# Performance work log

Measured on AMD Instinct MI355X. Metric: run time of the kernel, lower is better.

The kernel has to match this reference:

```python
import jax, jax.numpy as jnp
import numpy as np

DIM_Q = 512
DIM_K = 512
DIM_V = 512
NUM_HEADS = 8
TEMPERATURE = 0.1
LN_EPS = 1e-5


def setup_inputs() -> dict:
    key = jax.random.key(0)
    ks = jax.random.split(key, 12)
    B, n_q, n_k = 8, 1024, 1024
    s = 0.02
    return {
        "Q": jax.random.normal(ks[0], (B, n_q, DIM_Q), jnp.float32),
        "K": jax.random.normal(ks[1], (B, n_k, DIM_K), jnp.float32),
        "mask": jnp.ones((B, n_k), dtype=bool),
        "Wq": jax.random.normal(ks[2], (DIM_Q, DIM_V), jnp.float32) * s,
        "bq": jnp.zeros((DIM_V,), jnp.float32),
        "Wk": jax.random.normal(ks[3], (DIM_K, DIM_V), jnp.float32) * s,
        "bk": jnp.zeros((DIM_V,), jnp.float32),
        "Wv": jax.random.normal(ks[4], (DIM_K, DIM_V), jnp.float32) * s,
        "bv": jnp.zeros((DIM_V,), jnp.float32),
        "Wo": jax.random.normal(ks[5], (DIM_V, DIM_V), jnp.float32) * s,
        "bo": jnp.zeros((DIM_V,), jnp.float32),
        "gamma": jnp.ones((DIM_V,), jnp.float32),
        "beta": jnp.zeros((DIM_V,), jnp.float32),
    }


def _mab(Q, K, mask, Wq, bq, Wk, bk, Wv, bv, Wo, bo, gamma, beta):
    B, n_q, _ = Q.shape
    n_k = K.shape[1]
    H = NUM_HEADS
    d_head = DIM_V // H
    # projections, split heads: [B, H, n, d_head]
    Qh = (Q @ Wq + bq).reshape(B, n_q, H, d_head).transpose(0, 2, 1, 3)
    Kh = (K @ Wk + bk).reshape(B, n_k, H, d_head).transpose(0, 2, 1, 3)
    Vh = (K @ Wv + bv).reshape(B, n_k, H, d_head).transpose(0, 2, 1, 3)
    scale = 1.0 / (np.sqrt(d_head) * TEMPERATURE)
    A = jnp.einsum("bhqd,bhkd->bhqk", Qh, Kh) * scale
    A = jnp.where(mask[:, None, None, :], A, -jnp.inf)
    A = jax.nn.softmax(A, axis=-1)
    O = jnp.einsum("bhqk,bhkd->bhqd", A, Vh)
    O = O.transpose(0, 2, 1, 3).reshape(B, n_q, DIM_V)
    # fused output FFN + residual + LN
    O = O + jax.nn.relu(O @ Wo + bo)
    mu = jnp.mean(O, axis=-1, keepdims=True)
    var = jnp.var(O, axis=-1, keepdims=True)
    return (O - mu) * jax.lax.rsqrt(var + LN_EPS) * gamma + beta


def reference(Q, K, mask, Wq, bq, Wk, bk, Wv, bv, Wo, bo, gamma, beta):
    return _mab(Q, K, mask, Wq, bq, Wk, bk, Wv, bv, Wo, bo, gamma, beta)
```

## Files before the change

kernel.cpp:

```cpp
#include <hip/hip_runtime.h>

typedef __bf16 bf16;
typedef bf16 bf16x4 __attribute__((ext_vector_type(4)));
typedef bf16 bf16x8 __attribute__((ext_vector_type(8)));
typedef float floatx4 __attribute__((ext_vector_type(4)));

#define NB 8
#define NQ 1024
#define NK 1024
#define DIM 512
#define NH 8
#define DH 64

__device__ __forceinline__ void async16(const void* g, void* l) {
    __builtin_amdgcn_global_load_lds(
        (const __attribute__((address_space(1))) unsigned int*)(unsigned long long)(g),
        (__attribute__((address_space(3))) unsigned int*)(unsigned long long)(l),
        16, 0, 0);
}

__global__ __launch_bounds__(256) void prep_fused(
    const float* __restrict__ Q, const float* __restrict__ K,
    const float* __restrict__ Wq, const float* __restrict__ Wk,
    const float* __restrict__ Wv, const float* __restrict__ Wo,
    bf16* __restrict__ Qb, bf16* __restrict__ Kb, bf16* __restrict__ Wt)
{
    __shared__ bf16 Tl[64][68];
    const int bid = blockIdx.x;
    if (bid < 4096) {
        const int i = bid * 256 + threadIdx.x;
        float4 a = ((const float4*)Q)[i];
        float4 c = ((const float4*)K)[i];
        bf16x4 qa = {(bf16)a.x, (bf16)a.y, (bf16)a.z, (bf16)a.w};
        bf16x4 ka = {(bf16)c.x, (bf16)c.y, (bf16)c.z, (bf16)c.w};
        *(bf16x4*)(Qb + (size_t)i * 4) = qa;
        *(bf16x4*)(Kb + (size_t)i * 4) = ka;
    } else {
        const int bid2 = bid - 4096;
        const int w = bid2 >> 6;
        const int bx = bid2 & 7, by = (bid2 >> 3) & 7;
        const float* W = (w == 0) ? Wq : (w == 1) ? Wk : (w == 2) ? Wv : Wo;
        bf16* out = Wt + (size_t)w * DIM * DIM;
        const int k0 = bx * 64, n0 = by * 64;
        const int tx = threadIdx.x & 15, ty = threadIdx.x >> 4;
        for (int pass = 0; pass < 4; ++pass) {
            int k = ty + pass * 16;
            float4 v = *(const float4*)&W[(size_t)(k0 + k) * DIM + n0 + tx * 4];
            Tl[tx * 4 + 0][k] = (bf16)v.x;
            Tl[tx * 4 + 1][k] = (bf16)v.y;
            Tl[tx * 4 + 2][k] = (bf16)v.z;
            Tl[tx * 4 + 3][k] = (bf16)v.w;
        }
        __syncthreads();
        for (int pass = 0; pass < 4; ++pass) {
            int n = ty + pass * 16;
            bf16x4 ov = *(const bf16x4*)&Tl[n][tx * 4];
            *(bf16x4*)&out[(size_t)(n0 + n) * DIM + k0 + tx * 4] = ov;
        }
    }
}

__global__ __launch_bounds__(256) void proj_fused(
    const bf16* __restrict__ Qb, const bf16* __restrict__ Kb,
    const bf16* __restrict__ Wt,
    const float* __restrict__ bq, const float* __restrict__ bk,
    const float* __restrict__ bv,
    bf16* __restrict__ Qp, bf16* __restrict__ Kp, bf16* __restrict__ Vpt)
{
    __shared__ __attribute__((aligned(16))) bf16 sh[24576];
    const int t = threadIdx.x;
    const int wave = t >> 6, lane = t & 63, quad = lane >> 4, l16 = lane & 15;
    const int wr = wave >> 1, wc = wave & 1;
    const int bid = blockIdx.x;
    const bool isQ = bid < 512;
    const bf16* A; const bf16* W; int m0, n0;
    if (isQ) { A = Qb; W = Wt;             m0 = (bid & 63) * 128;  n0 = (bid >> 6) * 64; }
    else     { int b2 = bid - 512;
               A = Kb; W = Wt + 512 * DIM; m0 = (b2 & 63) * 128;   n0 = (b2 >> 6) * 64; }

    const int r1 = t >> 3, s1 = t & 7;
    const int p1 = s1 ^ (r1 & 7);
    const bf16* aSrc = A + (size_t)(m0 + r1) * DIM + p1 * 8;
    const bf16* wSrc = W + (size_t)(n0 + r1) * DIM + p1 * 8;

    floatx4 acc[4][2];
    for (int i = 0; i < 4; ++i)
        for (int j = 0; j < 2; ++j) acc[i][j] = (floatx4){0.f, 0.f, 0.f, 0.f};

    #pragma unroll
    for (int j = 0; j < 4; ++j)
        async16(aSrc + (size_t)j * 32 * DIM, sh + (t + j * 256) * 8);
    #pragma unroll
    for (int j = 0; j < 2; ++j)
        async16(wSrc + (size_t)j * 32 * DIM, sh + 16384 + (t + j * 256) * 8);

    for (int kt = 0; kt < 8; ++kt) {
        __syncthreads();
        const int cur = kt & 1;
        bf16* Acur = sh + cur * 8192;
        bf16* Bcur = sh + 16384 + cur * 4096;
        if (kt < 7) {
            bf16* Anxt = sh + (1 - cur) * 8192;
            bf16* Bnxt = sh + 16384 + (1 - cur) * 4096;
            const int ko = (kt + 1) * 64;
            #pragma unroll
            for (int j = 0; j < 4; ++j)
                async16(aSrc + ko + (size_t)j * 32 * DIM, Anxt + (t + j * 256) * 8);
            #pragma unroll
            for (int j = 0; j < 2; ++j)
                async16(wSrc + ko + (size_t)j * 32 * DIM, Bnxt + (t + j * 256) * 8);
        }
        #pragma unroll
        for (int ks = 0; ks < 2; ++ks) {
            bf16x8 af[4], bfr[2];
            #pragma unroll
            for (int mi = 0; mi < 4; ++mi) {
                const int row = wr * 64 + mi * 16 + l16;
                af[mi] = *(const bf16x8*)(Acur + row * 64 + (((ks * 4 + quad) ^ (row & 7)) << 3));
            }
            #pragma unroll
            for (int ni = 0; ni < 2; ++ni) {
                const int row = wc * 32 + ni * 16 + l16;
                bfr[ni] = *(const bf16x8*)(Bcur + row * 64 + (((ks * 4 + quad) ^ (row & 7)) << 3));
            }
            #pragma unroll
            for (int mi = 0; mi < 4; ++mi)
                #pragma unroll
                for (int ni = 0; ni < 2; ++ni)
                    acc[mi][ni] = __builtin_amdgcn_mfma_f32_16x16x32_bf16(
                        af[mi], bfr[ni], acc[mi][ni], 0, 0, 0);
        }
    }

    const bool isV = (!isQ) && (n0 >= 512);
    if (!isV) {
        bf16* out = isQ ? Qp : Kp;
        const float* bias = isQ ? bq : bk;
        const float qscale = isQ ? 1.8033688f : 1.0f;
        for (int ni = 0; ni < 2; ++ni) {
            const int n = n0 + wc * 32 + ni * 16 + l16;
            const float bb = bias[n];
            const int hd = n >> 6, d = n & 63;
            for (int mi = 0; mi < 4; ++mi) {
                for (int r = 0; r < 4; ++r) {
                    const int m = m0 + wr * 64 + mi * 16 + quad * 4 + r;
                    const int b = m >> 10, q = m & 1023;
                    out[((size_t)(b * 8 + hd) * 1024 + q) * 64 + d] =
                        (bf16)((acc[mi][ni][r] + bb) * qscale);
                }
            }
        }
    } else {
        __syncthreads();
        for (int ni = 0; ni < 2; ++ni) {
            const int n = wc * 32 + ni * 16 + l16;
            const float bb = bv[n0 + n - 512];
            for (int mi = 0; mi < 4; ++mi) {
                const int mb = wr * 64 + mi * 16 + quad * 4;
                const int slot = ((mb >> 3) ^ (n & 15));
                bf16x4 pk = {(bf16)(acc[mi][ni][0] + bb), (bf16)(acc[mi][ni][1] + bb),
                             (bf16)(acc[mi][ni][2] + bb), (bf16)(acc[mi][ni][3] + bb)};
                *(bf16x4*)(sh + n * 128 + slot * 8 + (mb & 7)) = pk;
            }
        }
        __syncthreads();
        const int n = t >> 2, hf = t & 3;
        const int nv = n0 + n - 512, hd = nv >> 6, d = nv & 63;
        const int b = m0 >> 10, qb = m0 & 1023;
        bf16* dst = Vpt + ((size_t)(b * 8 + hd) * 64 + d) * 1024 + qb;
        #pragma unroll
        for (int j = 0; j < 4; ++j) {
            const int ch = hf * 4 + j;
            const int slot = ch ^ (n & 15);
            bf16x8 v8 = *(const bf16x8*)(sh + n * 128 + slot * 8);
            *(bf16x8*)(dst + ch * 8) = v8;
        }
    }
}

__global__ __launch_bounds__(256, 4) void attn_kernel(
    const bf16* __restrict__ Qp, const bf16* __restrict__ Kp,
    const bf16* __restrict__ Vpt, const int* __restrict__ mask,
    bf16* __restrict__ Oa)
{
    const int bh = blockIdx.x & 63, qblk = blockIdx.x >> 6;
    const int b = bh >> 3, hd = bh & 7;
    const int t = threadIdx.x;
    const int wave = t >> 6, lane = t & 63, quad = lane >> 4, l16 = lane & 15;
    const int wq = wave >> 1, wk = wave & 1;

    __shared__ __attribute__((aligned(16))) bf16 Kt[2][64 * 64];
    __shared__ __attribute__((aligned(16))) bf16 Vt[2][64 * 64];
    __shared__ __attribute__((aligned(16))) bf16 Pl[4][32 * 32];

    const bf16* Qbase = Qp + ((size_t)bh * NQ + qblk * 64 + wq * 32) * DH;
    const bf16* Kbase = Kp + (size_t)bh * NK * DH;
    const bf16* Vbase = Vpt + (size_t)bh * DH * NK;
    const int* mrow = mask + b * NK;

    bf16x8 qf[2][2];
    #pragma unroll
    for (int qg = 0; qg < 2; ++qg)
        #pragma unroll
        for (int hh = 0; hh < 2; ++hh)
            qf[qg][hh] = *(const bf16x8*)(Qbase + (size_t)(qg * 16 + l16) * DH + hh * 32 + quad * 8);

    bf16x8 onesv;
    #pragma unroll
    for (int j = 0; j < 8; ++j) onesv[j] = (bf16)1.0f;

    floatx4 o[2][4];
    floatx4 osum[2];
    #pragma unroll
    for (int qg = 0; qg < 2; ++qg) {
        osum[qg] = (floatx4){0.f, 0.f, 0.f, 0.f};
        #pragma unroll
        for (int i = 0; i < 4; ++i) o[qg][i] = (floatx4){0.f, 0.f, 0.f, 0.f};
    }

    const int r1 = t >> 3, s1 = t & 7;
    const int p1 = s1 ^ (r1 & 7);
    const bf16* kSrc = Kbase + r1 * 64 + p1 * 8;
    const bf16* vSrc = Vbase + (size_t)r1 * 1024 + p1 * 8;

    async16(kSrc, Kt[0] + t * 8);
    async16(kSrc + 32 * 64, Kt[0] + (t + 256) * 8);
    async16(vSrc, Vt[0] + t * 8);
    async16(vSrc + (size_t)32 * 1024, Vt[0] + (t + 256) * 8);

    const int xor3 = (l16 & 3) ^ ((l16 >> 2) & 3);

    for (int kt = 0; kt < NK / 64; ++kt) {
        __syncthreads();
        const int cur = kt & 1;
        if (kt < NK / 64 - 1) {
            const int nxt = 1 - cur;
            async16(kSrc + (kt + 1) * 4096, Kt[nxt] + t * 8);
            async16(kSrc + (kt + 1) * 4096 + 32 * 64, Kt[nxt] + (t + 256) * 8);
            async16(vSrc + (kt + 1) * 64, Vt[nxt] + t * 8);
            async16(vSrc + (kt + 1) * 64 + (size_t)32 * 1024, Vt[nxt] + (t + 256) * 8);
        }

        bf16x8 kb[2][2];
        #pragma unroll
        for (int sub = 0; sub < 2; ++sub) {
            const int rowk = wk * 32 + sub * 16 + l16;
            kb[sub][0] = *(const bf16x8*)(Kt[cur] + rowk * 64 + ((quad ^ (rowk & 7)) << 3));
            kb[sub][1] = *(const bf16x8*)(Kt[cur] + rowk * 64 + (((quad + 4) ^ (rowk & 7)) << 3));
        }
        floatx4 sf[2][2];
        __builtin_amdgcn_s_setprio(1);
        #pragma unroll
        for (int sub = 0; sub < 2; ++sub)
            #pragma unroll
            for (int qg = 0; qg < 2; ++qg) {
                floatx4 s = {0.f, 0.f, 0.f, 0.f};
                s = __builtin_amdgcn_mfma_f32_16x16x32_bf16(kb[sub][0], qf[qg][0], s, 0, 0, 0);
                s = __builtin_amdgcn_mfma_f32_16x16x32_bf16(kb[sub][1], qf[qg][1], s, 0, 0, 0);
                sf[sub][qg] = s;
            }
        __builtin_amdgcn_s_setprio(0);

        const int mv = mrow[kt * 64 + lane];
        if (!__all(mv != 0)) {
            #pragma unroll
            for (int sub = 0; sub < 2; ++sub) {
                const int4 m4 = *(const int4*)&mrow[kt * 64 + wk * 32 + sub * 16 + quad * 4];
                #pragma unroll
                for (int qg = 0; qg < 2; ++qg) {
                    if (!m4.x) sf[sub][qg][0] = -3.0e38f;
                    if (!m4.y) sf[sub][qg][1] = -3.0e38f;
                    if (!m4.z) sf[sub][qg][2] = -3.0e38f;
                    if (!m4.w) sf[sub][qg][3] = -3.0e38f;
                }
            }
        }
        #pragma unroll
        for (int sub = 0; sub < 2; ++sub)
            #pragma unroll
            for (int qg = 0; qg < 2; ++qg) {
                bf16x4 pk = {(bf16)__builtin_amdgcn_exp2f(sf[sub][qg][0]),
                             (bf16)__builtin_amdgcn_exp2f(sf[sub][qg][1]),
                             (bf16)__builtin_amdgcn_exp2f(sf[sub][qg][2]),
                             (bf16)__builtin_amdgcn_exp2f(sf[sub][qg][3])};
                const int slot = (sub * 2 + (quad >> 1)) ^ xor3;
                *(bf16x4*)&Pl[wave][(qg * 16 + l16) * 32 + slot * 8 + (quad & 1) * 4] = pk;
            }
        bf16x8 af[2];
        #pragma unroll
        for (int qg = 0; qg < 2; ++qg)
            af[qg] = *(const bf16x8*)&Pl[wave][(qg * 16 + l16) * 32 + ((quad ^ xor3) << 3)];

        __builtin_amdgcn_s_setprio(1);
        osum[0] = __builtin_amdgcn_mfma_f32_16x16x32_bf16(af[0], onesv, osum[0], 0, 0, 0);
        osum[1] = __builtin_amdgcn_mfma_f32_16x16x32_bf16(af[1], onesv, osum[1], 0, 0, 0);
        #pragma unroll
        for (int dsub = 0; dsub < 4; ++dsub) {
            const int d = dsub * 16 + l16;
            bf16x8 vb = *(const bf16x8*)(Vt[cur] + d * 64 + (((wk * 4 + quad) ^ (d & 7)) << 3));
            o[0][dsub] = __builtin_amdgcn_mfma_f32_16x16x32_bf16(af[0], vb, o[0][dsub], 0, 0, 0);
            o[1][dsub] = __builtin_amdgcn_mfma_f32_16x16x32_bf16(af[1], vb, o[1][dsub], 0, 0, 0);
        }
        __builtin_amdgcn_s_setprio(0);
    }

    __syncthreads();
    float* scr  = (float*)Kt;
    float* scrL = (float*)Vt;

    {
        float* reg = scr + wave * 1024;
        if (wk == 0) {
            #pragma unroll
            for (int dsub = 0; dsub < 4; ++dsub)
                *(floatx4*)(reg + dsub * 256 + lane * 4) = o[1][dsub];
            if (l16 == 0) {
                #pragma unroll
                for (int r = 0; r < 4; ++r)
                    scrL[wave * 16 + quad * 4 + r] = osum[1][r];
            }
        } else {
            #pragma unroll
            for (int dsub = 0; dsub < 4; ++dsub)
                *(floatx4*)(reg + dsub * 256 + lane * 4) = o[0][dsub];
            if (l16 == 0) {
                #pragma unroll
                for (int r = 0; r < 4; ++r)
                    scrL[wave * 16 + quad * 4 + r] = osum[0][r];
            }
        }
    }
    __syncthreads();
    {
        const int partner = wq * 2 + (1 - wk);
        float* reg = scr + partner * 1024;
        floatx4 oo[4];
        floatx4 os;
        if (wk == 0) {
            oo[0] = o[0][0]; oo[1] = o[0][1]; oo[2] = o[0][2]; oo[3] = o[0][3];
            os = osum[0];
        } else {
            oo[0] = o[1][0]; oo[1] = o[1][1]; oo[2] = o[1][2]; oo[3] = o[1][3];
            os = osum[1];
        }
        #pragma unroll
        for (int dsub = 0; dsub < 4; ++dsub)
            oo[dsub] += *(const floatx4*)(reg + dsub * 256 + lane * 4);
        float linv[4];
        #pragma unroll
        for (int r = 0; r < 4; ++r)
            linv[r] = 1.f / (os[r] + scrL[partner * 16 + quad * 4 + r]);
        for (int dsub = 0; dsub < 4; ++dsub) {
            for (int r = 0; r < 4; ++r) {
                const int q = qblk * 64 + wq * 32 + wk * 16 + quad * 4 + r;
                const int col = hd * 64 + dsub * 16 + l16;
                Oa[((size_t)(b * NQ + q)) * DIM + col] = (bf16)(oo[dsub][r] * linv[r]);
            }
        }
    }
}

__global__ __launch_bounds__(256) void ffn_gemm(
    const bf16* __restrict__ Oa, const bf16* __restrict__ W,
    const float* __restrict__ bias, bf16* __restrict__ Yb)
{
    __shared__ __attribute__((aligned(16))) bf16 sh[32768];
    const int t = threadIdx.x;
    const int wave = t >> 6, lane = t & 63, quad = lane >> 4, l16 = lane & 15;
    const int wr = wave >> 1, wc = wave & 1;
    const int m0 = (blockIdx.x & 63) * 128, n0 = (blockIdx.x >> 6) * 64;
    const int ktr = n0 >> 6;

    const int r1 = t >> 3, s1 = t & 7;
    const int p1 = s1 ^ (r1 & 7);
    const bf16* aSrc = Oa + (size_t)(m0 + r1) * DIM + p1 * 8;
    const bf16* wSrc = W  + (size_t)(n0 + r1) * DIM + p1 * 8;

    floatx4 acc[4][2];
    for (int i = 0; i < 4; ++i)
        for (int j = 0; j < 2; ++j) acc[i][j] = (floatx4){0.f, 0.f, 0.f, 0.f};

    #pragma unroll
    for (int j = 0; j < 4; ++j)
        async16(aSrc + (size_t)j * 32 * DIM, sh + (t + j * 256) * 8);
    #pragma unroll
    for (int j = 0; j < 2; ++j)
        async16(wSrc + (size_t)j * 32 * DIM, sh + 16384 + (t + j * 256) * 8);

    for (int kt = 0; kt < 8; ++kt) {
        __syncthreads();
        const int cur = kt & 1;
        bf16* Acur = sh + cur * 8192;
        bf16* Bcur = sh + 16384 + cur * 4096;
        if (kt < 7) {
            bf16* Anxt = sh + (1 - cur) * 8192;
            bf16* Bnxt = sh + 16384 + (1 - cur) * 4096;
            const int ko = (kt + 1) * 64;
            #pragma unroll
            for (int j = 0; j < 4; ++j)
                async16(aSrc + ko + (size_t)j * 32 * DIM, Anxt + (t + j * 256) * 8);
            #pragma unroll
            for (int j = 0; j < 2; ++j)
                async16(wSrc + ko + (size_t)j * 32 * DIM, Bnxt + (t + j * 256) * 8);
        }
        if (kt == ktr) {
            #pragma unroll
            for (int j = 0; j < 4; ++j) {
                const int idx = t + j * 256;
                *(bf16x8*)(sh + 24576 + idx * 8) = *(const bf16x8*)(Acur + idx * 8);
            }
        }
        #pragma unroll
        for (int ks = 0; ks < 2; ++ks) {
            bf16x8 af[4], bfr[2];
            #pragma unroll
            for (int mi = 0; mi < 4; ++mi) {
                const int row = wr * 64 + mi * 16 + l16;
                af[mi] = *(const bf16x8*)(Acur + row * 64 + (((ks * 4 + quad) ^ (row & 7)) << 3));
            }
            #pragma unroll
            for (int ni = 0; ni < 2; ++ni) {
                const int row = wc * 32 + ni * 16 + l16;
                bfr[ni] = *(const bf16x8*)(Bcur + row * 64 + (((ks * 4 + quad) ^ (row & 7)) << 3));
            }
            #pragma unroll
            for (int mi = 0; mi < 4; ++mi)
                #pragma unroll
                for (int ni = 0; ni < 2; ++ni)
                    acc[mi][ni] = __builtin_amdgcn_mfma_f32_16x16x32_bf16(
                        af[mi], bfr[ni], acc[mi][ni], 0, 0, 0);
        }
    }
    __syncthreads();

    for (int ni = 0; ni < 2; ++ni) {
        const int n = n0 + wc * 32 + ni * 16 + l16;
        const int cl = wc * 32 + ni * 16 + l16;
        const int chi = cl >> 3, clo = cl & 7;
        const float bb = bias[n];
        for (int mi = 0; mi < 4; ++mi) {
            for (int r = 0; r < 4; ++r) {
                const int rl = wr * 64 + mi * 16 + quad * 4 + r;
                const float ov = (float)sh[24576 + rl * 64 + ((chi ^ (rl & 7)) << 3) + clo];
                Yb[(size_t)(m0 + rl) * DIM + n] = (bf16)(ov + fmaxf(acc[mi][ni][r] + bb, 0.f));
            }
        }
    }
}

__global__ __launch_bounds__(256) void ln_kernel(
    const bf16* __restrict__ Y, const float* __restrict__ gamma,
    const float* __restrict__ beta, float* __restrict__ out)
{
    const int row  = blockIdx.x * 4 + (threadIdx.x >> 6);
    const int lane = threadIdx.x & 63;
    bf16x8 v = *(const bf16x8*)(Y + (size_t)row * DIM + lane * 8);
    float f[8];
    float s = 0.f, sq = 0.f;
    #pragma unroll
    for (int j = 0; j < 8; ++j) {
        f[j] = (float)v[j];
        s += f[j];
        sq += f[j] * f[j];
    }
    for (int mk = 32; mk >= 1; mk >>= 1) {
        s  += __shfl_xor(s,  mk, 64);
        sq += __shfl_xor(sq, mk, 64);
    }
    const float mu  = s * (1.f / 512.f);
    const float var = sq * (1.f / 512.f) - mu * mu;
    const float inv = rsqrtf(var + 1e-5f);
    float4 g1 = ((const float4*)gamma)[lane * 2];
    float4 g2 = ((const float4*)gamma)[lane * 2 + 1];
    float4 b1 = ((const float4*)beta)[lane * 2];
    float4 b2 = ((const float4*)beta)[lane * 2 + 1];
    float4 o1, o2;
    o1.x = (f[0] - mu) * inv * g1.x + b1.x;
    o1.y = (f[1] - mu) * inv * g1.y + b1.y;
    o1.z = (f[2] - mu) * inv * g1.z + b1.z;
    o1.w = (f[3] - mu) * inv * g1.w + b1.w;
    o2.x = (f[4] - mu) * inv * g2.x + b2.x;
    o2.y = (f[5] - mu) * inv * g2.y + b2.y;
    o2.z = (f[6] - mu) * inv * g2.z + b2.z;
    o2.w = (f[7] - mu) * inv * g2.w + b2.w;
    float* orow = out + (size_t)row * DIM;
    ((float4*)orow)[lane * 2]     = o1;
    ((float4*)orow)[lane * 2 + 1] = o2;
}

extern "C" void kernel_launch(void* const* d_in, const int* in_sizes, int n_in,
                              void* d_out, int out_size, void* d_ws, size_t ws_size,
                              hipStream_t stream) {
    const float* Q  = (const float*)d_in[0];
    const float* K  = (const float*)d_in[1];
    const int*   mask = (const int*)d_in[2];
    const float* Wq = (const float*)d_in[3];
    const float* bq = (const float*)d_in[4];
    const float* Wk = (const float*)d_in[5];
    const float* bk = (const float*)d_in[6];
    const float* Wv = (const float*)d_in[7];
    const float* bv = (const float*)d_in[8];
    const float* Wo = (const float*)d_in[9];
    const float* bo = (const float*)d_in[10];
    const float* gamma = (const float*)d_in[11];
    const float* beta  = (const float*)d_in[12];

    char* ws = (char*)d_ws;
    bf16* Wt  = (bf16*)(ws);
    bf16* Qb  = (bf16*)(ws + 2097152);
    bf16* Kb  = (bf16*)(ws + 10485760);
    bf16* Qp  = (bf16*)(ws + 18874368);
    bf16* Kp  = (bf16*)(ws + 27262976);
    bf16* Vpt = (bf16*)(ws + 35651584);
    bf16* Oa  = (bf16*)(ws + 44040192);
    bf16* Yb  = (bf16*)(ws + 52428800);
    float* out = (float*)d_out;

    prep_fused<<<4352, 256, 0, stream>>>(Q, K, Wq, Wk, Wv, Wo, Qb, Kb, Wt);
    proj_fused<<<1536, 256, 0, stream>>>(Qb, Kb, Wt, bq, bk, bv, Qp, Kp, Vpt);
    attn_kernel<<<1024, 256, 0, stream>>>(Qp, Kp, Vpt, mask, Oa);
    ffn_gemm<<<512, 256, 0, stream>>>(Oa, Wt + 3 * 262144, bo, Yb);
    ln_kernel<<<2048, 256, 0, stream>>>(Yb, gamma, beta, out);
}
```

Measured before the change: 162.5 us.

## Fuse fp32-to-bf16 conversion of Q and K into projection GEMM loads

Removes the separate elementwise pass that converted Q and K to bf16 in the workspace. The projection kernel now loads fp32 activation tiles into registers, converts them, and writes swizzled bf16 into shared memory, prefetching the next tile across the MFMA loop. This drops one full write plus re-read of 16 MB of intermediate data. In exchange the A-tile loads become synchronous register loads that take more VGPRs, and each K tile is reread as fp32 by the eight column blocks that share it.

```diff
diff --git a/kernel.cpp b/kernel.cpp
--- a/kernel.cpp
+++ b/kernel.cpp
@@ -20,48 +20,36 @@
 }
 
 __global__ __launch_bounds__(256) void prep_fused(
-    const float* __restrict__ Q, const float* __restrict__ K,
     const float* __restrict__ Wq, const float* __restrict__ Wk,
     const float* __restrict__ Wv, const float* __restrict__ Wo,
-    bf16* __restrict__ Qb, bf16* __restrict__ Kb, bf16* __restrict__ Wt)
+    bf16* __restrict__ Wt)
 {
     __shared__ bf16 Tl[64][68];
-    const int bid = blockIdx.x;
-    if (bid < 4096) {
-        const int i = bid * 256 + threadIdx.x;
-        float4 a = ((const float4*)Q)[i];
-        float4 c = ((const float4*)K)[i];
-        bf16x4 qa = {(bf16)a.x, (bf16)a.y, (bf16)a.z, (bf16)a.w};
-        bf16x4 ka = {(bf16)c.x, (bf16)c.y, (bf16)c.z, (bf16)c.w};
-        *(bf16x4*)(Qb + (size_t)i * 4) = qa;
-        *(bf16x4*)(Kb + (size_t)i * 4) = ka;
-    } else {
-        const int bid2 = bid - 4096;
-        const int w = bid2 >> 6;
-        const int bx = bid2 & 7, by = (bid2 >> 3) & 7;
-        const float* W = (w == 0) ? Wq : (w == 1) ? Wk : (w == 2) ? Wv : Wo;
-        bf16* out = Wt + (size_t)w * DIM * DIM;
-        const int k0 = bx * 64, n0 = by * 64;
-        const int tx = threadIdx.x & 15, ty = threadIdx.x >> 4;
-        for (int pass = 0; pass < 4; ++pass) {
-            int k = ty + pass * 16;
-            float4 v = *(const float4*)&W[(size_t)(k0 + k) * DIM + n0 + tx * 4];
-            Tl[tx * 4 + 0][k] = (bf16)v.x;
-            Tl[tx * 4 + 1][k] = (bf16)v.y;
-            Tl[tx * 4 + 2][k] = (bf16)v.z;
-            Tl[tx * 4 + 3][k] = (bf16)v.w;
-        }
-        __syncthreads();
-        for (int pass = 0; pass < 4; ++pass) {
-            int n = ty + pass * 16;
-            bf16x4 ov = *(const bf16x4*)&Tl[n][tx * 4];
-            *(bf16x4*)&out[(size_t)(n0 + n) * DIM + k0 + tx * 4] = ov;
-        }
+    const int bid2 = blockIdx.x;
+    const int w = bid2 >> 6;
+    const int bx = bid2 & 7, by = (bid2 >> 3) & 7;
+    const float* W = (w == 0) ? Wq : (w == 1) ? Wk : (w == 2) ? Wv : Wo;
+    bf16* out = Wt + (size_t)w * DIM * DIM;
+    const int k0 = bx * 64, n0 = by * 64;
+    const int tx = threadIdx.x & 15, ty = threadIdx.x >> 4;
+    for (int pass = 0; pass < 4; ++pass) {
+        int k = ty + pass * 16;
+        float4 v = *(const float4*)&W[(size_t)(k0 + k) * DIM + n0 + tx * 4];
+        Tl[tx * 4 + 0][k] = (bf16)v.x;
+        Tl[tx * 4 + 1][k] = (bf16)v.y;
+        Tl[tx * 4 + 2][k] = (bf16)v.z;
+        Tl[tx * 4 + 3][k] = (bf16)v.w;
+    }
+    __syncthreads();
+    for (int pass = 0; pass < 4; ++pass) {
+        int n = ty + pass * 16;
+        bf16x4 ov = *(const bf16x4*)&Tl[n][tx * 4];
+        *(bf16x4*)&out[(size_t)(n0 + n) * DIM + k0 + tx * 4] = ov;
     }
 }
 
 __global__ __launch_bounds__(256) void proj_fused(
-    const bf16* __restrict__ Qb, const bf16* __restrict__ Kb,
+    const float* __restrict__ Qf, const float* __restrict__ Kf,
     const bf16* __restrict__ Wt,
     const float* __restrict__ bq, const float* __restrict__ bk,
     const float* __restrict__ bv,
@@ -73,26 +61,36 @@
     const int wr = wave >> 1, wc = wave & 1;
     const int bid = blockIdx.x;
     const bool isQ = bid < 512;
-    const bf16* A; const bf16* W; int m0, n0;
-    if (isQ) { A = Qb; W = Wt;             m0 = (bid & 63) * 128;  n0 = (bid >> 6) * 64; }
+    const float* A; const bf16* W; int m0, n0;
+    if (isQ) { A = Qf; W = Wt;             m0 = (bid & 63) * 128;  n0 = (bid >> 6) * 64; }
     else     { int b2 = bid - 512;
-               A = Kb; W = Wt + 512 * DIM; m0 = (b2 & 63) * 128;   n0 = (b2 >> 6) * 64; }
+               A = Kf; W = Wt + 512 * DIM; m0 = (b2 & 63) * 128;   n0 = (b2 >> 6) * 64; }
 
     const int r1 = t >> 3, s1 = t & 7;
     const int p1 = s1 ^ (r1 & 7);
-    const bf16* aSrc = A + (size_t)(m0 + r1) * DIM + p1 * 8;
-    const bf16* wSrc = W + (size_t)(n0 + r1) * DIM + p1 * 8;
+    const float* aSrc = A + (size_t)(m0 + r1) * DIM + p1 * 8;
+    const bf16*  wSrc = W + (size_t)(n0 + r1) * DIM + p1 * 8;
 
     floatx4 acc[4][2];
     for (int i = 0; i < 4; ++i)
         for (int j = 0; j < 2; ++j) acc[i][j] = (floatx4){0.f, 0.f, 0.f, 0.f};
 
-    #pragma unroll
-    for (int j = 0; j < 4; ++j)
-        async16(aSrc + (size_t)j * 32 * DIM, sh + (t + j * 256) * 8);
+    float4 la[4][2];
+
     #pragma unroll
     for (int j = 0; j < 2; ++j)
         async16(wSrc + (size_t)j * 32 * DIM, sh + 16384 + (t + j * 256) * 8);
+    #pragma unroll
+    for (int j = 0; j < 4; ++j) {
+        la[j][0] = *(const float4*)(aSrc + (size_t)j * 32 * DIM);
+        la[j][1] = *(const float4*)(aSrc + (size_t)j * 32 * DIM + 4);
+    }
+    #pragma unroll
+    for (int j = 0; j < 4; ++j) {
+        bf16x8 w8 = {(bf16)la[j][0].x, (bf16)la[j][0].y, (bf16)la[j][0].z, (bf16)la[j][0].w,
+                     (bf16)la[j][1].x, (bf16)la[j][1].y, (bf16)la[j][1].z, (bf16)la[j][1].w};
+        *(bf16x8*)(sh + (t + j * 256) * 8) = w8;
+    }
 
     for (int kt = 0; kt < 8; ++kt) {
         __syncthreads();
@@ -100,15 +98,16 @@
         bf16* Acur = sh + cur * 8192;
         bf16* Bcur = sh + 16384 + cur * 4096;
         if (kt < 7) {
-            bf16* Anxt = sh + (1 - cur) * 8192;
             bf16* Bnxt = sh + 16384 + (1 - cur) * 4096;
             const int ko = (kt + 1) * 64;
             #pragma unroll
-            for (int j = 0; j < 4; ++j)
-                async16(aSrc + ko + (size_t)j * 32 * DIM, Anxt + (t + j * 256) * 8);
-            #pragma unroll
             for (int j = 0; j < 2; ++j)
                 async16(wSrc + ko + (size_t)j * 32 * DIM, Bnxt + (t + j * 256) * 8);
+            #pragma unroll
+            for (int j = 0; j < 4; ++j) {
+                la[j][0] = *(const float4*)(aSrc + ko + (size_t)j * 32 * DIM);
+                la[j][1] = *(const float4*)(aSrc + ko + (size_t)j * 32 * DIM + 4);
+            }
         }
         #pragma unroll
         for (int ks = 0; ks < 2; ++ks) {
@@ -129,6 +128,15 @@
                 for (int ni = 0; ni < 2; ++ni)
                     acc[mi][ni] = __builtin_amdgcn_mfma_f32_16x16x32_bf16(
                         af[mi], bfr[ni], acc[mi][ni], 0, 0, 0);
+        }
+        if (kt < 7) {
+            bf16* Anxt = sh + (1 - cur) * 8192;
+            #pragma unroll
+            for (int j = 0; j < 4; ++j) {
+                bf16x8 w8 = {(bf16)la[j][0].x, (bf16)la[j][0].y, (bf16)la[j][0].z, (bf16)la[j][0].w,
+                             (bf16)la[j][1].x, (bf16)la[j][1].y, (bf16)la[j][1].z, (bf16)la[j][1].w};
+                *(bf16x8*)(Anxt + (t + j * 256) * 8) = w8;
+            }
         }
     }
 
@@ -507,8 +515,6 @@
 
     char* ws = (char*)d_ws;
     bf16* Wt  = (bf16*)(ws);
-    bf16* Qb  = (bf16*)(ws + 2097152);
-    bf16* Kb  = (bf16*)(ws + 10485760);
     bf16* Qp  = (bf16*)(ws + 18874368);
     bf16* Kp  = (bf16*)(ws + 27262976);
     bf16* Vpt = (bf16*)(ws + 35651584);
@@ -516,8 +522,8 @@
     bf16* Yb  = (bf16*)(ws + 52428800);
     float* out = (float*)d_out;
 
-    prep_fused<<<4352, 256, 0, stream>>>(Q, K, Wq, Wk, Wv, Wo, Qb, Kb, Wt);
-    proj_fused<<<1536, 256, 0, stream>>>(Qb, Kb, Wt, bq, bk, bv, Qp, Kp, Vpt);
+    prep_fused<<<256, 256, 0, stream>>>(Wq, Wk, Wv, Wo, Wt);
+    proj_fused<<<1536, 256, 0, stream>>>(Q, K, Wt, bq, bk, bv, Qp, Kp, Vpt);
     attn_kernel<<<1024, 256, 0, stream>>>(Qp, Kp, Vpt, mask, Oa);
     ffn_gemm<<<512, 256, 0, stream>>>(Oa, Wt + 3 * 262144, bo, Yb);
     ln_kernel<<<2048, 256, 0, stream>>>(Yb, gamma, beta, out);
```

After: 169.2 us. +4.1%, slower.

## Keep softmax probabilities in registers via transposed 16x16x16 MFMA for PV

Applied to the files above, without the earlier changes.

Drops the per-wave LDS round trip for the probability tile. The PV product is now computed transposed (O^T = V^T P^T) with 16x16x16 bf16 MFMAs, so the exponentiated score fragments feed the B operand directly from registers. The V tile reads and the row-sum MFMA are re-indexed to match. Because the output is now laid out with rows along lanes, the epilogue writes 4 contiguous bf16 per lane instead of scalar stores. The trade-off is twice as many MFMA instructions of half the K depth, plus narrower 8-byte LDS reads of V.

```diff
diff --git a/kernel.cpp b/kernel.cpp
--- a/kernel.cpp
+++ b/kernel.cpp
@@ -4,6 +4,7 @@
 typedef bf16 bf16x4 __attribute__((ext_vector_type(4)));
 typedef bf16 bf16x8 __attribute__((ext_vector_type(8)));
 typedef float floatx4 __attribute__((ext_vector_type(4)));
+typedef short short4i __attribute__((ext_vector_type(4)));
 
 #define NB 8
 #define NQ 1024
@@ -17,6 +18,19 @@
         (const __attribute__((address_space(1))) unsigned int*)(unsigned long long)(g),
         (__attribute__((address_space(3))) unsigned int*)(unsigned long long)(l),
         16, 0, 0);
+}
+
+__device__ __forceinline__ floatx4 mfma_16x16x16(bf16x4 a, bf16x4 b, floatx4 c) {
+#if __has_builtin(__builtin_amdgcn_mfma_f32_16x16x16_bf16)
+    return __builtin_amdgcn_mfma_f32_16x16x16_bf16(a, b, c, 0, 0, 0);
+#elif __has_builtin(__builtin_amdgcn_mfma_f32_16x16x16bf16_1k)
+    return __builtin_amdgcn_mfma_f32_16x16x16bf16_1k(
+        __builtin_bit_cast(short4i, a), __builtin_bit_cast(short4i, b), c, 0, 0, 0);
+#else
+    asm volatile("v_mfma_f32_16x16x16_bf16 %0, %1, %2, %0\n\ts_nop 7\n\ts_nop 7"
+                 : "+v"(c) : "v"(a), "v"(b));
+    return c;
+#endif
 }
 
 __global__ __launch_bounds__(256) void prep_fused(
@@ -191,7 +205,6 @@
 
     __shared__ __attribute__((aligned(16))) bf16 Kt[2][64 * 64];
     __shared__ __attribute__((aligned(16))) bf16 Vt[2][64 * 64];
-    __shared__ __attribute__((aligned(16))) bf16 Pl[4][32 * 32];
 
     const bf16* Qbase = Qp + ((size_t)bh * NQ + qblk * 64 + wq * 32) * DH;
     const bf16* Kbase = Kp + (size_t)bh * NK * DH;
@@ -205,9 +218,9 @@
         for (int hh = 0; hh < 2; ++hh)
             qf[qg][hh] = *(const bf16x8*)(Qbase + (size_t)(qg * 16 + l16) * DH + hh * 32 + quad * 8);
 
-    bf16x8 onesv;
-    #pragma unroll
-    for (int j = 0; j < 8; ++j) onesv[j] = (bf16)1.0f;
+    bf16x4 ones4;
+    #pragma unroll
+    for (int j = 0; j < 4; ++j) ones4[j] = (bf16)1.0f;
 
     floatx4 o[2][4];
     floatx4 osum[2];
@@ -227,8 +240,6 @@
     async16(kSrc + 32 * 64, Kt[0] + (t + 256) * 8);
     async16(vSrc, Vt[0] + t * 8);
     async16(vSrc + (size_t)32 * 1024, Vt[0] + (t + 256) * 8);
-
-    const int xor3 = (l16 & 3) ^ ((l16 >> 2) & 3);
 
     for (int kt = 0; kt < NK / 64; ++kt) {
         __syncthreads();
@@ -275,32 +286,31 @@
                 }
             }
         }
+        bf16x4 pb[2][2];
         #pragma unroll
         for (int sub = 0; sub < 2; ++sub)
             #pragma unroll
-            for (int qg = 0; qg < 2; ++qg) {
-                bf16x4 pk = {(bf16)__builtin_amdgcn_exp2f(sf[sub][qg][0]),
-                             (bf16)__builtin_amdgcn_exp2f(sf[sub][qg][1]),
-                             (bf16)__builtin_amdgcn_exp2f(sf[sub][qg][2]),
-                             (bf16)__builtin_amdgcn_exp2f(sf[sub][qg][3])};
-                const int slot = (sub * 2 + (quad >> 1)) ^ xor3;
-                *(bf16x4*)&Pl[wave][(qg * 16 + l16) * 32 + slot * 8 + (quad & 1) * 4] = pk;
-            }
-        bf16x8 af[2];
-        #pragma unroll
-        for (int qg = 0; qg < 2; ++qg)
-            af[qg] = *(const bf16x8*)&Pl[wave][(qg * 16 + l16) * 32 + ((quad ^ xor3) << 3)];
+            for (int qg = 0; qg < 2; ++qg)
+                pb[sub][qg] = (bf16x4){(bf16)__builtin_amdgcn_exp2f(sf[sub][qg][0]),
+                                       (bf16)__builtin_amdgcn_exp2f(sf[sub][qg][1]),
+                                       (bf16)__builtin_amdgcn_exp2f(sf[sub][qg][2]),
+                                       (bf16)__builtin_amdgcn_exp2f(sf[sub][qg][3])};
 
         __builtin_amdgcn_s_setprio(1);
-        osum[0] = __builtin_amdgcn_mfma_f32_16x16x32_bf16(af[0], onesv, osum[0], 0, 0, 0);
-        osum[1] = __builtin_amdgcn_mfma_f32_16x16x32_bf16(af[1], onesv, osum[1], 0, 0, 0);
-        #pragma unroll
-        for (int dsub = 0; dsub < 4; ++dsub) {
-            const int d = dsub * 16 + l16;
-            bf16x8 vb = *(const bf16x8*)(Vt[cur] + d * 64 + (((wk * 4 + quad) ^ (d & 7)) << 3));
-            o[0][dsub] = __builtin_amdgcn_mfma_f32_16x16x32_bf16(af[0], vb, o[0][dsub], 0, 0, 0);
-            o[1][dsub] = __builtin_amdgcn_mfma_f32_16x16x32_bf16(af[1], vb, o[1][dsub], 0, 0, 0);
-        }
+        osum[0] = mfma_16x16x16(ones4, pb[0][0], osum[0]);
+        osum[0] = mfma_16x16x16(ones4, pb[1][0], osum[0]);
+        osum[1] = mfma_16x16x16(ones4, pb[0][1], osum[1]);
+        osum[1] = mfma_16x16x16(ones4, pb[1][1], osum[1]);
+        #pragma unroll
+        for (int sub = 0; sub < 2; ++sub)
+            #pragma unroll
+            for (int dsub = 0; dsub < 4; ++dsub) {
+                const int d = dsub * 16 + l16;
+                bf16x4 av = *(const bf16x4*)(Vt[cur] + d * 64 +
+                    (((wk * 8 + sub * 4 + quad) ^ ((d & 7) << 1)) << 2));
+                o[0][dsub] = mfma_16x16x16(av, pb[sub][0], o[0][dsub]);
+                o[1][dsub] = mfma_16x16x16(av, pb[sub][1], o[1][dsub]);
+            }
         __builtin_amdgcn_s_setprio(0);
     }
 
@@ -314,20 +324,12 @@
             #pragma unroll
             for (int dsub = 0; dsub < 4; ++dsub)
                 *(floatx4*)(reg + dsub * 256 + lane * 4) = o[1][dsub];
-            if (l16 == 0) {
-                #pragma unroll
-                for (int r = 0; r < 4; ++r)
-                    scrL[wave * 16 + quad * 4 + r] = osum[1][r];
-            }
+            if (quad == 0) scrL[wave * 16 + l16] = osum[1][0];
         } else {
             #pragma unroll
             for (int dsub = 0; dsub < 4; ++dsub)
                 *(floatx4*)(reg + dsub * 256 + lane * 4) = o[0][dsub];
-            if (l16 == 0) {
-                #pragma unroll
-                for (int r = 0; r < 4; ++r)
-                    scrL[wave * 16 + quad * 4 + r] = osum[0][r];
-            }
+            if (quad == 0) scrL[wave * 16 + l16] = osum[0][0];
         }
     }
     __syncthreads();
@@ -335,27 +337,25 @@
         const int partner = wq * 2 + (1 - wk);
         float* reg = scr + partner * 1024;
         floatx4 oo[4];
-        floatx4 os;
+        float os;
         if (wk == 0) {
             oo[0] = o[0][0]; oo[1] = o[0][1]; oo[2] = o[0][2]; oo[3] = o[0][3];
-            os = osum[0];
+            os = osum[0][0];
         } else {
             oo[0] = o[1][0]; oo[1] = o[1][1]; oo[2] = o[1][2]; oo[3] = o[1][3];
-            os = osum[1];
+            os = osum[1][0];
         }
         #pragma unroll
         for (int dsub = 0; dsub < 4; ++dsub)
             oo[dsub] += *(const floatx4*)(reg + dsub * 256 + lane * 4);
-        float linv[4];
-        #pragma unroll
-        for (int r = 0; r < 4; ++r)
-            linv[r] = 1.f / (os[r] + scrL[partner * 16 + quad * 4 + r]);
+        const float linv = 1.f / (os + scrL[partner * 16 + l16]);
+        const int q = qblk * 64 + wq * 32 + wk * 16 + l16;
+        bf16* orow = Oa + ((size_t)(b * NQ + q)) * DIM + hd * 64;
+        #pragma unroll
         for (int dsub = 0; dsub < 4; ++dsub) {
-            for (int r = 0; r < 4; ++r) {
-                const int q = qblk * 64 + wq * 32 + wk * 16 + quad * 4 + r;
-                const int col = hd * 64 + dsub * 16 + l16;
-                Oa[((size_t)(b * NQ + q)) * DIM + col] = (bf16)(oo[dsub][r] * linv[r]);
-            }
+            bf16x4 st = {(bf16)(oo[dsub][0] * linv), (bf16)(oo[dsub][1] * linv),
+                         (bf16)(oo[dsub][2] * linv), (bf16)(oo[dsub][3] * linv)};
+            *(bf16x4*)(orow + dsub * 16 + quad * 4) = st;
         }
     }
 }
```

Result: no change. 164.2 us (+1.0%).
